# Performance work log

Measured on AMD Instinct MI355X. Metric: run time of the kernel, lower is better.

The kernel has to match this reference:

```python
import jax, jax.numpy as jnp
import numpy as np

N_HEAD = 16


def setup_inputs() -> dict:
    key = jax.random.key(0)
    ks = jax.random.split(key, 6)
    b, l, d = 4, 2048, 1024
    n_mem = 1000  # FAISS index is populated with 1000 random vectors per batch element
    return {
        "q": jax.random.normal(ks[0], (b, l, d), dtype=jnp.float32),
        "kv": jax.random.normal(ks[1], (b, l, d), dtype=jnp.float32),  # unused by forward (faithful)
        "mem_table": jax.random.uniform(ks[2], (b, n_mem, d), dtype=jnp.float32),
        "w_q": jax.random.normal(ks[3], (d, d), dtype=jnp.float32) / np.sqrt(d),
        "w_kv": jax.random.normal(ks[4], (d, 2 * (d // N_HEAD)), dtype=jnp.float32) / np.sqrt(d),
        "w_concat": jax.random.normal(ks[5], (d, d), dtype=jnp.float32) / np.sqrt(d),
        "topk": 1,
    }


def reference(q, kv, mem_table, w_q, w_kv, w_concat, topk):
    b, l, d = q.shape
    h = N_HEAD
    dh = d // h

    qp = q @ w_q  # (b, l, d)

    # Exact inner-product kNN (topk=1) replacing the per-batch FAISS HNSW search:
    # brute-force scores + argmax + gather of the nearest memory vector.
    knn_scores = jnp.einsum("bld,bnd->bln", qp, mem_table)  # (b, l, n_mem)
    idx = jnp.argmax(knn_scores, axis=-1)  # (b, l) int
    mem = jnp.take_along_axis(mem_table, idx[..., None], axis=1)  # (b, l, d)

    k, v = jnp.split(mem @ w_kv, 2, axis=-1)  # each (b, l, dh)

    qh = qp.reshape(b, l, h, dh).transpose(0, 2, 1, 3)  # (b, h, l, dh)
    # k, v are shared across heads (unsqueeze(1) in torch -> broadcast here)
    att = jnp.einsum("bhld,bmd->bhlm", qh, k) / np.float32(np.sqrt(dh))  # (b, h, l, l)
    att = jax.nn.softmax(att, axis=-1)
    out = jnp.einsum("bhlm,bmd->bhld", att, v)  # (b, h, l, dh)

    out = out.transpose(0, 2, 1, 3).reshape(b, l, d)
    return out @ w_concat
```

## Files before the change

kernel.cpp:

```cpp
#include <hip/hip_runtime.h>
#include <float.h>
#include <math.h>

#define BATCH 4
#define SEQ   2048
#define DIM   1024
#define NHEAD 16
#define DHEAD 64
#define NMEM  1000
#define NPAD  1024
#define ROWS  (BATCH*SEQ)
#define QSCALE 0.18033688011112042f

typedef __attribute__((ext_vector_type(8))) __bf16 bf16x8;
typedef __attribute__((ext_vector_type(4))) __bf16 bf16x4;
typedef __attribute__((ext_vector_type(4))) float  f32x4;

static __device__ inline f32x4 mfma16(bf16x8 a, bf16x8 b, f32x4 c) {
  return __builtin_amdgcn_mfma_f32_16x16x32_bf16(a, b, c, 0, 0, 0);
}

#define GLOAD16(g, l) __builtin_amdgcn_global_load_lds( \
    (const __attribute__((address_space(1))) unsigned int*)(g), \
    (__attribute__((address_space(3))) unsigned int*)(l), 16, 0, 0)

enum { MODE_C = 0, MODE_HILO = 1, MODE_ARGMAX = 2, MODE_KV = 3 };

template<int AF32, int NPROD, int MODE>
__global__ __launch_bounds__(256) void gemm3(
    const void* __restrict__ Ah_, const __bf16* __restrict__ Al,
    const __bf16* __restrict__ Bh, const __bf16* __restrict__ Bl,
    int rowsPerZ, long bStrideZ,
    float* __restrict__ C, __bf16* __restrict__ Oh, __bf16* __restrict__ Ol,
    float* __restrict__ pv, int* __restrict__ pi)
{
  extern __shared__ char smem[];
  __shared__ float s_pv[128];
  __shared__ int   s_pi[128];
  const int t = threadIdx.x;
  const int w = t >> 6, lane = t & 63, l15 = lane & 15, g = lane >> 4;
  const int wr = w >> 1, wc = w & 1;
  const int m0 = blockIdx.z * rowsPerZ + blockIdx.x * 128;
  const int n0 = blockIdx.y * 128;
  const __bf16* Bh_b = Bh + (size_t)blockIdx.z * bStrideZ;
  const __bf16* Bl_b = (NPROD == 3) ? (Bl + (size_t)blockIdx.z * bStrideZ) : (const __bf16*)0;

  constexpr int SB = (AF32 || NPROD == 3) ? 32768 : 16384;
  constexpr int BOFF = AF32 ? 16384 : (NPROD == 3 ? 16384 : 8192);

  f32x4 acc[4][4];
  #pragma unroll
  for (int i = 0; i < 4; ++i)
    #pragma unroll
    for (int j = 0; j < 4; ++j) acc[i][j] = (f32x4){0.f, 0.f, 0.f, 0.f};

  auto STAGE = [&](int buf, int k0) {
    char* base = smem + buf * SB;
    if (AF32) {
      const float* Af = (const float*)Ah_;
      #pragma unroll
      for (int i = 0; i < 4; ++i) {
        int c = i * 256 + t;
        int r = c >> 3, s = c & 7;
        int sl = s ^ (r & 7);
        GLOAD16(&Af[(size_t)(m0 + r) * DIM + k0 + sl * 4], base + i * 4096 + w * 1024);
      }
    } else {
      const __bf16* Ab = (const __bf16*)Ah_;
      #pragma unroll
      for (int i = 0; i < 2; ++i) {
        int c = i * 256 + t;
        int r = c >> 2, s = c & 3;
        int sl = s ^ (r & 3);
        GLOAD16(&Ab[(size_t)(m0 + r) * DIM + k0 + sl * 8], base + i * 4096 + w * 1024);
        if (NPROD == 3)
          GLOAD16(&Al[(size_t)(m0 + r) * DIM + k0 + sl * 8], base + 8192 + i * 4096 + w * 1024);
      }
    }
    char* bB = base + BOFF;
    #pragma unroll
    for (int i = 0; i < 2; ++i) {
      int c = i * 256 + t;
      int r = c >> 2, s = c & 3;
      int sl = s ^ (r & 3);
      GLOAD16(&Bh_b[(size_t)(n0 + r) * DIM + k0 + sl * 8], bB + i * 4096 + w * 1024);
      if (NPROD == 3)
        GLOAD16(&Bl_b[(size_t)(n0 + r) * DIM + k0 + sl * 8], bB + 8192 + i * 4096 + w * 1024);
    }
  };

  STAGE(0, 0);
  __syncthreads();
  int cur = 0;

  for (int k0 = 0; k0 < DIM; k0 += 32) {
    if (k0 + 32 < DIM) STAGE(cur ^ 1, k0 + 32);

    char* base = smem + cur * SB;
    char* sA   = base;
    char* sAl  = base + 8192;
    char* sBh  = base + BOFF;
    char* sBl  = sBh + 8192;

    bf16x8 ah[4], al[4], bh[4], bl[4];
    #pragma unroll
    for (int mi = 0; mi < 4; ++mi) {
      int r = wr * 64 + mi * 16 + l15;
      if (AF32) {
        int p0 = (2 * g) ^ (r & 7), p1 = (2 * g + 1) ^ (r & 7);
        float4 q0 = *(const float4*)(sA + r * 128 + p0 * 16);
        float4 q1 = *(const float4*)(sA + r * 128 + p1 * 16);
        float qq[8] = {q0.x, q0.y, q0.z, q0.w, q1.x, q1.y, q1.z, q1.w};
        #pragma unroll
        for (int j = 0; j < 8; ++j) {
          __bf16 h = (__bf16)qq[j];
          ah[mi][j] = h;
          al[mi][j] = (__bf16)(qq[j] - (float)h);
        }
      } else {
        int p = (g ^ (r & 3)) * 16;
        ah[mi] = *(const bf16x8*)(sA + r * 64 + p);
        if (NPROD == 3) al[mi] = *(const bf16x8*)(sAl + r * 64 + p);
      }
    }
    #pragma unroll
    for (int ni = 0; ni < 4; ++ni) {
      int r = wc * 64 + ni * 16 + l15;
      int p = (g ^ (r & 3)) * 16;
      bh[ni] = *(const bf16x8*)(sBh + r * 64 + p);
      if (NPROD == 3) bl[ni] = *(const bf16x8*)(sBl + r * 64 + p);
    }
    __builtin_amdgcn_s_setprio(1);
    #pragma unroll
    for (int mi = 0; mi < 4; ++mi)
      #pragma unroll
      for (int ni = 0; ni < 4; ++ni) {
        acc[mi][ni] = mfma16(ah[mi], bh[ni], acc[mi][ni]);
        if (NPROD == 3) {
          acc[mi][ni] = mfma16(ah[mi], bl[ni], acc[mi][ni]);
          acc[mi][ni] = mfma16(al[mi], bh[ni], acc[mi][ni]);
        }
      }
    __builtin_amdgcn_s_setprio(0);
    __syncthreads();
    cur ^= 1;
  }

  if (MODE == MODE_C) {
    #pragma unroll
    for (int mi = 0; mi < 4; ++mi)
      #pragma unroll
      for (int ni = 0; ni < 4; ++ni) {
        int col = n0 + wc * 64 + ni * 16 + l15;
        #pragma unroll
        for (int r = 0; r < 4; ++r) {
          int row = m0 + wr * 64 + mi * 16 + g * 4 + r;
          C[(size_t)row * DIM + col] = acc[mi][ni][r];
        }
      }
  } else if (MODE == MODE_HILO) {
    #pragma unroll
    for (int mi = 0; mi < 4; ++mi)
      #pragma unroll
      for (int ni = 0; ni < 4; ++ni) {
        int col = n0 + wc * 64 + ni * 16 + l15;
        #pragma unroll
        for (int r = 0; r < 4; ++r) {
          int row = m0 + wr * 64 + mi * 16 + g * 4 + r;
          float v = acc[mi][ni][r] * QSCALE;
          __bf16 h = (__bf16)v;
          Oh[(size_t)row * DIM + col] = h;
          Ol[(size_t)row * DIM + col] = (__bf16)(v - (float)h);
        }
      }
  } else if (MODE == MODE_KV) {
    #pragma unroll
    for (int mi = 0; mi < 4; ++mi)
      #pragma unroll
      for (int ni = 0; ni < 4; ++ni) {
        int col = wc * 64 + ni * 16 + l15;
        #pragma unroll
        for (int r = 0; r < 4; ++r) {
          int gr = m0 + wr * 64 + mi * 16 + g * 4 + r;
          int bb = gr >> 10, n = gr & (NPAD - 1);
          __bf16 h = (__bf16)acc[mi][ni][r];
          if (col < DHEAD) {
            Oh[(size_t)gr * DHEAD + col] = h;
          } else {
            int np = (n & ~63) | ((n & 15) << 2) | ((n >> 4) & 3);
            Ol[((size_t)bb * DHEAD + (col - DHEAD)) * NPAD + np] = h;
          }
        }
      }
  } else {
    float vv[4][4]; int ii[4][4];
    #pragma unroll
    for (int mi = 0; mi < 4; ++mi)
      #pragma unroll
      for (int r = 0; r < 4; ++r) {
        float v = -FLT_MAX; int vi = 0x7fffffff;
        #pragma unroll
        for (int ni = 0; ni < 4; ++ni) {
          int col = n0 + wc * 64 + ni * 16 + l15;
          float s = (col < NMEM) ? acc[mi][ni][r] : -FLT_MAX;
          if (s > v) { v = s; vi = col; }
        }
        #pragma unroll
        for (int off = 1; off < 16; off <<= 1) {
          float ov = __shfl_xor(v, off);
          int   oi = __shfl_xor(vi, off);
          if (ov > v || (ov == v && oi < vi)) { v = ov; vi = oi; }
        }
        vv[mi][r] = v; ii[mi][r] = vi;
        if (wc == 0 && l15 == 0) {
          int lrow = wr * 64 + mi * 16 + g * 4 + r;
          s_pv[lrow] = v; s_pi[lrow] = vi;
        }
      }
    __syncthreads();
    if (wc == 1 && l15 == 0) {
      #pragma unroll
      for (int mi = 0; mi < 4; ++mi)
        #pragma unroll
        for (int r = 0; r < 4; ++r) {
          int lrow = wr * 64 + mi * 16 + g * 4 + r;
          float v0 = s_pv[lrow]; int i0 = s_pi[lrow];
          float v1 = vv[mi][r];  int i1 = ii[mi][r];
          float v; int vi;
          if (v1 > v0) { v = v1; vi = i1; } else { v = v0; vi = i0; }
          pv[(size_t)blockIdx.y * ROWS + m0 + lrow] = v;
          pi[(size_t)blockIdx.y * ROWS + m0 + lrow] = vi;
        }
    }
  }
}

__global__ __launch_bounds__(256) void knn_reduce(const float* __restrict__ pv,
                                                  const int* __restrict__ pi,
                                                  int* __restrict__ idx) {
  int r = blockIdx.x * 256 + threadIdx.x;
  float bv = -FLT_MAX; int bi = 0x7fffffff;
  #pragma unroll
  for (int c = 0; c < 8; ++c) {
    float v = pv[(size_t)c * ROWS + r];
    int   i = pi[(size_t)c * ROWS + r];
    if (v > bv || (v == bv && i < bi)) { bv = v; bi = i; }
  }
  idx[r] = bi;
}

__global__ __launch_bounds__(256) void hist_lc(const int* __restrict__ idx,
                                               float* __restrict__ lc) {
  __shared__ int hcnt[NPAD];
  const int t = threadIdx.x, b = blockIdx.x;
  #pragma unroll
  for (int i = 0; i < 4; ++i) hcnt[t + 256 * i] = 0;
  __syncthreads();
  #pragma unroll
  for (int i = 0; i < 8; ++i) atomicAdd(&hcnt[idx[b * SEQ + i * 256 + t]], 1);
  __syncthreads();
  #pragma unroll
  for (int i = 0; i < 4; ++i) {
    int n = t + 256 * i;
    int c = hcnt[n];
    lc[b * NPAD + n] = (n < NMEM && c > 0) ? log2f((float)c) : -1e30f;
  }
}

__global__ __launch_bounds__(256) void attn_table(const __bf16* __restrict__ qph,
                                                  const __bf16* __restrict__ Ktab,
                                                  const __bf16* __restrict__ VtTp,
                                                  const float* __restrict__ lc2,
                                                  __bf16* __restrict__ attn_bf) {
  extern __shared__ char smem[];
  char* sK = smem;
  char* sV = smem + 16384;
  char* sP = smem + 32768;

  const int t = threadIdx.x;
  const int wq = t >> 6, lane = t & 63, l15 = lane & 15, g = lane >> 4;
  const int b = blockIdx.z, h = blockIdx.y;
  const int q0 = blockIdx.x * 256 + wq * 64;

  bf16x8 qa[4][2];
  #pragma unroll
  for (int mi = 0; mi < 4; ++mi)
    #pragma unroll
    for (int ks = 0; ks < 2; ++ks)
      qa[mi][ks] = *(const bf16x8*)&qph[(size_t)(b * SEQ + q0 + mi * 16 + l15) * DIM +
                                        h * DHEAD + ks * 32 + g * 8];

  f32x4 O[4][4];
  #pragma unroll
  for (int mi = 0; mi < 4; ++mi)
    #pragma unroll
    for (int fd = 0; fd < 4; ++fd) O[mi][fd] = (f32x4){0.f, 0.f, 0.f, 0.f};
  float lsum[4][4];
  #pragma unroll
  for (int mi = 0; mi < 4; ++mi)
    #pragma unroll
    for (int r = 0; r < 4; ++r) lsum[mi][r] = 0.f;

  const __bf16* Kb = Ktab + (size_t)b * NPAD * DHEAD;
  const __bf16* Vb = VtTp + (size_t)b * DHEAD * NPAD;
  const float* lcb = lc2 + b * NPAD;
  char* sPw = sP + wq * 8192;

  auto STAGE = [&](int buf, int tile) {
    const int n0 = tile * 64;
    #pragma unroll
    for (int i = 0; i < 2; ++i) {
      int c = i * 256 + t, row = c >> 3, s = c & 7, sl = s ^ (row & 7);
      GLOAD16(&Kb[(size_t)(n0 + row) * DHEAD + sl * 8], sK + buf * 8192 + i * 4096 + wq * 1024);
      GLOAD16(&Vb[(size_t)row * NPAD + n0 + sl * 8], sV + buf * 8192 + i * 4096 + wq * 1024);
    }
  };

  STAGE(0, 0);
  __syncthreads();
  int cur = 0;

  for (int tile = 0; tile < NPAD / 64; ++tile) {
    if (tile + 1 < NPAD / 64) STAGE(cur ^ 1, tile + 1);

    const int n0 = tile * 64;
    float lcv[4];
    #pragma unroll
    for (int ni = 0; ni < 4; ++ni) lcv[ni] = lcb[n0 + ni * 16 + l15];

    bf16x8 kf[2][4];
    #pragma unroll
    for (int ks = 0; ks < 2; ++ks)
      #pragma unroll
      for (int ni = 0; ni < 4; ++ni)
        kf[ks][ni] = *(const bf16x8*)(sK + cur * 8192 + (ni * 16 + l15) * 128 +
                                      (((ks * 4 + g) ^ (l15 & 7)) * 16));

    #pragma unroll
    for (int mi = 0; mi < 4; ++mi) {
      f32x4 S[4];
      #pragma unroll
      for (int ni = 0; ni < 4; ++ni) S[ni] = (f32x4){0.f, 0.f, 0.f, 0.f};
      __builtin_amdgcn_s_setprio(1);
      #pragma unroll
      for (int ks = 0; ks < 2; ++ks)
        #pragma unroll
        for (int ni = 0; ni < 4; ++ni)
          S[ni] = mfma16(qa[mi][ks], kf[ks][ni], S[ni]);
      __builtin_amdgcn_s_setprio(0);
      #pragma unroll
      for (int r = 0; r < 4; ++r) {
        int row = mi * 16 + g * 4 + r;
        bf16x4 p4;
        float rs = 0.f;
        #pragma unroll
        for (int ni = 0; ni < 4; ++ni) {
          float p = __builtin_amdgcn_exp2f(S[ni][r] + lcv[ni]);
          rs += p;
          p4[ni] = (__bf16)p;
        }
        *(bf16x4*)(sPw + row * 128 + ((l15 * 8) ^ ((row & 7) << 4))) = p4;
        lsum[mi][r] += rs;
      }
    }

    #pragma unroll
    for (int ks = 0; ks < 2; ++ks) {
      bf16x8 vf[4];
      #pragma unroll
      for (int fd = 0; fd < 4; ++fd)
        vf[fd] = *(const bf16x8*)(sV + cur * 8192 + (fd * 16 + l15) * 128 +
                                  (((ks * 4 + g) ^ (l15 & 7)) * 16));
      __builtin_amdgcn_s_setprio(1);
      #pragma unroll
      for (int mi = 0; mi < 4; ++mi) {
        int row = mi * 16 + l15;
        bf16x8 pa = *(const bf16x8*)(sPw + row * 128 +
                                     ((ks * 64 + g * 16) ^ ((row & 7) << 4)));
        #pragma unroll
        for (int fd = 0; fd < 4; ++fd)
          O[mi][fd] = mfma16(pa, vf[fd], O[mi][fd]);
      }
      __builtin_amdgcn_s_setprio(0);
    }

    __syncthreads();
    cur ^= 1;
  }

  #pragma unroll
  for (int mi = 0; mi < 4; ++mi)
    #pragma unroll
    for (int r = 0; r < 4; ++r) {
      float rs = lsum[mi][r];
      #pragma unroll
      for (int off = 1; off < 16; off <<= 1) rs += __shfl_xor(rs, off);
      float inv = 1.f / rs;
      size_t row = (size_t)(b * SEQ + q0 + mi * 16 + g * 4 + r);
      #pragma unroll
      for (int fd = 0; fd < 4; ++fd)
        attn_bf[row * DIM + h * DHEAD + fd * 16 + l15] = (__bf16)(O[mi][fd][r] * inv);
    }
}

__global__ __launch_bounds__(256) void cast_w_t(const float* __restrict__ in,
                                                __bf16* __restrict__ oh,
                                                __bf16* __restrict__ ol,
                                                int writeLo) {
  __shared__ float tile[64][65];
  const int t = threadIdx.x;
  const int k0 = blockIdx.x * 64, n0 = blockIdx.y * 64;
  #pragma unroll
  for (int i = 0; i < 16; ++i) {
    int e = t + i * 256, r = e >> 6, c = e & 63;
    tile[r][c] = in[(size_t)(k0 + r) * DIM + n0 + c];
  }
  __syncthreads();
  #pragma unroll
  for (int i = 0; i < 16; ++i) {
    int e = t + i * 256, r = e >> 6, c = e & 63;
    float v = tile[c][r];
    __bf16 h = (__bf16)v;
    oh[(size_t)(n0 + r) * DIM + k0 + c] = h;
    if (writeLo) ol[(size_t)(n0 + r) * DIM + k0 + c] = (__bf16)(v - (float)h);
  }
}

__global__ __launch_bounds__(256) void cast_wkv_t(const float* __restrict__ in,
                                                  __bf16* __restrict__ oh,
                                                  __bf16* __restrict__ ol) {
  __shared__ float tile[64][65];
  const int t = threadIdx.x;
  const int k0 = blockIdx.x * 64, n0 = blockIdx.y * 64;
  #pragma unroll
  for (int i = 0; i < 16; ++i) {
    int e = t + i * 256, r = e >> 6, c = e & 63;
    tile[r][c] = in[(size_t)(k0 + r) * 128 + n0 + c];
  }
  __syncthreads();
  #pragma unroll
  for (int i = 0; i < 16; ++i) {
    int e = t + i * 256, r = e >> 6, c = e & 63;
    float v = tile[c][r];
    __bf16 h = (__bf16)v;
    oh[(size_t)(n0 + r) * DIM + k0 + c] = h;
    ol[(size_t)(n0 + r) * DIM + k0 + c] = (__bf16)(v - (float)h);
  }
}

__global__ __launch_bounds__(256) void cast_mem(const float* __restrict__ mem,
                                                __bf16* __restrict__ mh,
                                                __bf16* __restrict__ ml) {
  size_t e = ((size_t)blockIdx.x * 256 + threadIdx.x) * 8;
  int d = (int)(e & 1023);
  size_t rn = e >> 10;
  int n = (int)(rn & 1023), b = (int)(rn >> 10);
  bf16x8 h8, l8;
  if (n < NMEM) {
    const float* p = mem + ((size_t)b * NMEM + n) * DIM + d;
    #pragma unroll
    for (int j = 0; j < 8; ++j) {
      float v = p[j];
      __bf16 h = (__bf16)v;
      h8[j] = h; l8[j] = (__bf16)(v - (float)h);
    }
  } else {
    #pragma unroll
    for (int j = 0; j < 8; ++j) { h8[j] = (__bf16)0.f; l8[j] = (__bf16)0.f; }
  }
  *(bf16x8*)(mh + e) = h8;
  *(bf16x8*)(ml + e) = l8;
}

extern "C" void kernel_launch(void* const* d_in, const int* in_sizes, int n_in,
                              void* d_out, int out_size, void* d_ws, size_t ws_size,
                              hipStream_t stream) {
  const float* q        = (const float*)d_in[0];
  const float* mem      = (const float*)d_in[2];
  const float* w_q      = (const float*)d_in[3];
  const float* w_kv     = (const float*)d_in[4];
  const float* w_concat = (const float*)d_in[5];
  float* out = (float*)d_out;

  char* wsb = (char*)d_ws;
  __bf16* memh   = (__bf16*)(wsb + 0);
  __bf16* meml   = (__bf16*)(wsb + 8388608);
  __bf16* wqt_h  = (__bf16*)(wsb + 16777216);
  __bf16* wqt_l  = (__bf16*)(wsb + 18874368);
  __bf16* wct    = (__bf16*)(wsb + 20971520);
  __bf16* Ktab   = (__bf16*)(wsb + 23068672);
  __bf16* VtT    = (__bf16*)(wsb + 23592960);
  float*  lc     = (float*) (wsb + 24117248);
  float*  pv     = (float*) (wsb + 24133632);
  int*    pi     = (int*)   (wsb + 24395776);
  int*    idx    = (int*)   (wsb + 24657920);
  __bf16* wkvT_h = (__bf16*)(wsb + 24690688);
  __bf16* wkvT_l = (__bf16*)(wsb + 24952832);
  __bf16* qph    = (__bf16*)(wsb + 25214976);
  __bf16* qpl    = (__bf16*)(wsb + 41992192);
  __bf16* attn_bf = qpl;

  cast_w_t<<<dim3(16, 16), 256, 0, stream>>>(w_q, wqt_h, wqt_l, 1);
  cast_w_t<<<dim3(16, 16), 256, 0, stream>>>(w_concat, wct, (__bf16*)0, 0);
  cast_wkv_t<<<dim3(16, 2), 256, 0, stream>>>(w_kv, wkvT_h, wkvT_l);
  cast_mem<<<dim3(2048), 256, 0, stream>>>(mem, memh, meml);

  gemm3<1, 3, MODE_HILO><<<dim3(64, 8, 1), 256, 65536, stream>>>(
      (const void*)q, (const __bf16*)0, wqt_h, wqt_l, 0, 0,
      (float*)0, qph, qpl, (float*)0, (int*)0);

  gemm3<0, 3, MODE_KV><<<dim3(BATCH * NPAD / 128, 1, 1), 256, 65536, stream>>>(
      (const void*)memh, meml, wkvT_h, wkvT_l, 0, 0,
      (float*)0, Ktab, VtT, (float*)0, (int*)0);

  gemm3<0, 3, MODE_ARGMAX><<<dim3(16, 8, 4), 256, 65536, stream>>>(
      (const void*)qph, qpl, memh, meml, 2048, (long)NPAD * DIM,
      (float*)0, (__bf16*)0, (__bf16*)0, pv, pi);
  knn_reduce<<<dim3(32), 256, 0, stream>>>(pv, pi, idx);

  hist_lc<<<dim3(BATCH), 256, 0, stream>>>(idx, lc);

  attn_table<<<dim3(SEQ / 256, NHEAD, BATCH), 256, 65536, stream>>>(
      qph, Ktab, VtT, lc, attn_bf);

  gemm3<0, 1, MODE_C><<<dim3(64, 8, 1), 256, 32768, stream>>>(
      (const void*)attn_bf, (const __bf16*)0, wct, (const __bf16*)0, 0, 0,
      out, (__bf16*)0, (__bf16*)0, (float*)0, (int*)0);
}
```

Baseline: 237.2 us.

## Use single-bf16 kNN scoring with top-2 candidates and fp32 rescoring

```diff
diff --git a/kernel.cpp b/kernel.cpp
--- a/kernel.cpp
+++ b/kernel.cpp
@@ -11,6 +11,7 @@
 #define NPAD  1024
 #define ROWS  (BATCH*SEQ)
 #define QSCALE 0.18033688011112042f
+#define RESCORE_DELTA 0.10f
 
 typedef __attribute__((ext_vector_type(8))) __bf16 bf16x8;
 typedef __attribute__((ext_vector_type(4))) __bf16 bf16x4;
@@ -35,8 +36,6 @@
     float* __restrict__ pv, int* __restrict__ pi)
 {
   extern __shared__ char smem[];
-  __shared__ float s_pv[128];
-  __shared__ int   s_pi[128];
   const int t = threadIdx.x;
   const int w = t >> 6, lane = t & 63, l15 = lane & 15, g = lane >> 4;
   const int wr = w >> 1, wc = w & 1;
@@ -193,60 +192,83 @@
         }
       }
   } else {
-    float vv[4][4]; int ii[4][4];
     #pragma unroll
     for (int mi = 0; mi < 4; ++mi)
       #pragma unroll
       for (int r = 0; r < 4; ++r) {
-        float v = -FLT_MAX; int vi = 0x7fffffff;
+        float v1 = -FLT_MAX, v2 = -FLT_MAX;
+        int   i1 = 0x7fffffff, i2 = 0x7fffffff;
         #pragma unroll
         for (int ni = 0; ni < 4; ++ni) {
           int col = n0 + wc * 64 + ni * 16 + l15;
           float s = (col < NMEM) ? acc[mi][ni][r] : -FLT_MAX;
-          if (s > v) { v = s; vi = col; }
+          if (s > v1 || (s == v1 && col < i1)) { v2 = v1; i2 = i1; v1 = s; i1 = col; }
+          else if (s > v2 || (s == v2 && col < i2)) { v2 = s; i2 = col; }
         }
         #pragma unroll
         for (int off = 1; off < 16; off <<= 1) {
-          float ov = __shfl_xor(v, off);
-          int   oi = __shfl_xor(vi, off);
-          if (ov > v || (ov == v && oi < vi)) { v = ov; vi = oi; }
-        }
-        vv[mi][r] = v; ii[mi][r] = vi;
-        if (wc == 0 && l15 == 0) {
-          int lrow = wr * 64 + mi * 16 + g * 4 + r;
-          s_pv[lrow] = v; s_pi[lrow] = vi;
-        }
-      }
-    __syncthreads();
-    if (wc == 1 && l15 == 0) {
-      #pragma unroll
-      for (int mi = 0; mi < 4; ++mi)
-        #pragma unroll
-        for (int r = 0; r < 4; ++r) {
-          int lrow = wr * 64 + mi * 16 + g * 4 + r;
-          float v0 = s_pv[lrow]; int i0 = s_pi[lrow];
-          float v1 = vv[mi][r];  int i1 = ii[mi][r];
-          float v; int vi;
-          if (v1 > v0) { v = v1; vi = i1; } else { v = v0; vi = i0; }
-          pv[(size_t)blockIdx.y * ROWS + m0 + lrow] = v;
-          pi[(size_t)blockIdx.y * ROWS + m0 + lrow] = vi;
-        }
-    }
-  }
-}
-
-__global__ __launch_bounds__(256) void knn_reduce(const float* __restrict__ pv,
-                                                  const int* __restrict__ pi,
-                                                  int* __restrict__ idx) {
-  int r = blockIdx.x * 256 + threadIdx.x;
-  float bv = -FLT_MAX; int bi = 0x7fffffff;
-  #pragma unroll
-  for (int c = 0; c < 8; ++c) {
-    float v = pv[(size_t)c * ROWS + r];
-    int   i = pi[(size_t)c * ROWS + r];
-    if (v > bv || (v == bv && i < bi)) { bv = v; bi = i; }
-  }
-  idx[r] = bi;
+          float w1 = __shfl_xor(v1, off), w2 = __shfl_xor(v2, off);
+          int   j1 = __shfl_xor(i1, off), j2 = __shfl_xor(i2, off);
+          if (w1 > v1 || (w1 == v1 && j1 < i1)) { v2 = v1; i2 = i1; v1 = w1; i1 = j1; }
+          else if (w1 > v2 || (w1 == v2 && j1 < i2)) { v2 = w1; i2 = j1; }
+          if (w2 > v1 || (w2 == v1 && j2 < i1)) { v2 = v1; i2 = i1; v1 = w2; i1 = j2; }
+          else if (w2 > v2 || (w2 == v2 && j2 < i2)) { v2 = w2; i2 = j2; }
+        }
+        if (l15 == 0) {
+          int row = m0 + wr * 64 + mi * 16 + g * 4 + r;
+          int half = blockIdx.y * 2 + wc;
+          pv[(size_t)(half * 2 + 0) * ROWS + row] = v1;
+          pv[(size_t)(half * 2 + 1) * ROWS + row] = v2;
+          pi[(size_t)(half * 2 + 0) * ROWS + row] = i1;
+          pi[(size_t)(half * 2 + 1) * ROWS + row] = i2;
+        }
+      }
+  }
+}
+
+__global__ __launch_bounds__(256) void knn_rescore(const __bf16* __restrict__ qph,
+                                                   const __bf16* __restrict__ qpl,
+                                                   const float* __restrict__ mem,
+                                                   const float* __restrict__ pv,
+                                                   const int* __restrict__ pi,
+                                                   int* __restrict__ idx) {
+  const int t = threadIdx.x;
+  const int wq = t >> 6, lane = t & 63;
+  const int qrow = blockIdx.x * 4 + wq;
+  const int batch = qrow >> 11;
+
+  float cv = (lane < 32) ? pv[(size_t)lane * ROWS + qrow] : -FLT_MAX;
+  int   ci = (lane < 32) ? pi[(size_t)lane * ROWS + qrow] : 0x7fffffff;
+
+  float M = cv;
+  #pragma unroll
+  for (int off = 1; off < 64; off <<= 1) M = fmaxf(M, __shfl_xor(M, off));
+
+  unsigned long long cand = __ballot(cv >= M - RESCORE_DELTA && ci < NMEM);
+
+  float qp[16];
+  {
+    const __bf16* ph = qph + (size_t)qrow * DIM + lane * 16;
+    const __bf16* pl = qpl + (size_t)qrow * DIM + lane * 16;
+    #pragma unroll
+    for (int j = 0; j < 16; ++j) qp[j] = (float)ph[j] + (float)pl[j];
+  }
+
+  float best = -FLT_MAX;
+  int besti = 0x7fffffff;
+  while (cand) {
+    int b = __ffsll((long long)cand) - 1;
+    cand &= cand - 1;
+    int c = __shfl(ci, b);
+    const float* mrow = mem + ((size_t)batch * NMEM + c) * DIM + lane * 16;
+    float part = 0.f;
+    #pragma unroll
+    for (int j = 0; j < 16; ++j) part = fmaf(qp[j], mrow[j], part);
+    #pragma unroll
+    for (int off = 1; off < 64; off <<= 1) part += __shfl_xor(part, off);
+    if (part > best || (part == best && c < besti)) { best = part; besti = c; }
+  }
+  if (lane == 0) idx[qrow] = besti;
 }
 
 __global__ __launch_bounds__(256) void hist_lc(const int* __restrict__ idx,
@@ -472,6 +494,23 @@
   *(bf16x8*)(ml + e) = l8;
 }
 
+__global__ __launch_bounds__(256) void cast_q(const float* __restrict__ q,
+                                              __bf16* __restrict__ qh,
+                                              __bf16* __restrict__ ql) {
+  size_t e = ((size_t)blockIdx.x * 256 + threadIdx.x) * 8;
+  float4 a = *(const float4*)(q + e);
+  float4 b = *(const float4*)(q + e + 4);
+  float vv[8] = {a.x, a.y, a.z, a.w, b.x, b.y, b.z, b.w};
+  bf16x8 h8, l8;
+  #pragma unroll
+  for (int j = 0; j < 8; ++j) {
+    __bf16 h = (__bf16)vv[j];
+    h8[j] = h; l8[j] = (__bf16)(vv[j] - (float)h);
+  }
+  *(bf16x8*)(qh + e) = h8;
+  *(bf16x8*)(ql + e) = l8;
+}
+
 extern "C" void kernel_launch(void* const* d_in, const int* in_sizes, int n_in,
                               void* d_out, int out_size, void* d_ws, size_t ws_size,
                               hipStream_t stream) {
@@ -492,31 +531,35 @@
   __bf16* VtT    = (__bf16*)(wsb + 23592960);
   float*  lc     = (float*) (wsb + 24117248);
   float*  pv     = (float*) (wsb + 24133632);
-  int*    pi     = (int*)   (wsb + 24395776);
-  int*    idx    = (int*)   (wsb + 24657920);
-  __bf16* wkvT_h = (__bf16*)(wsb + 24690688);
-  __bf16* wkvT_l = (__bf16*)(wsb + 24952832);
-  __bf16* qph    = (__bf16*)(wsb + 25214976);
-  __bf16* qpl    = (__bf16*)(wsb + 41992192);
+  int*    pi     = (int*)   (wsb + 25182208);
+  int*    idx    = (int*)   (wsb + 26230784);
+  __bf16* wkvT_h = (__bf16*)(wsb + 26263552);
+  __bf16* wkvT_l = (__bf16*)(wsb + 26525696);
+  __bf16* qph    = (__bf16*)(wsb + 26787840);
+  __bf16* qpl    = (__bf16*)(wsb + 43565056);
   __bf16* attn_bf = qpl;
+  __bf16* qh = (__bf16*)d_out;
+  __bf16* ql = (__bf16*)d_out + (size_t)ROWS * DIM;
 
   cast_w_t<<<dim3(16, 16), 256, 0, stream>>>(w_q, wqt_h, wqt_l, 1);
   cast_w_t<<<dim3(16, 16), 256, 0, stream>>>(w_concat, wct, (__bf16*)0, 0);
   cast_wkv_t<<<dim3(16, 2), 256, 0, stream>>>(w_kv, wkvT_h, wkvT_l);
   cast_mem<<<dim3(2048), 256, 0, stream>>>(mem, memh, meml);
-
-  gemm3<1, 3, MODE_HILO><<<dim3(64, 8, 1), 256, 65536, stream>>>(
-      (const void*)q, (const __bf16*)0, wqt_h, wqt_l, 0, 0,
+  cast_q<<<dim3(4096), 256, 0, stream>>>(q, qh, ql);
+
+  gemm3<0, 3, MODE_HILO><<<dim3(64, 8, 1), 256, 65536, stream>>>(
+      (const void*)qh, ql, wqt_h, wqt_l, 0, 0,
       (float*)0, qph, qpl, (float*)0, (int*)0);
 
   gemm3<0, 3, MODE_KV><<<dim3(BATCH * NPAD / 128, 1, 1), 256, 65536, stream>>>(
       (const void*)memh, meml, wkvT_h, wkvT_l, 0, 0,
       (float*)0, Ktab, VtT, (float*)0, (int*)0);
 
-  gemm3<0, 3, MODE_ARGMAX><<<dim3(16, 8, 4), 256, 65536, stream>>>(
-      (const void*)qph, qpl, memh, meml, 2048, (long)NPAD * DIM,
+  gemm3<0, 1, MODE_ARGMAX><<<dim3(16, 8, 4), 256, 32768, stream>>>(
+      (const void*)qph, (const __bf16*)0, memh, (const __bf16*)0, 2048, (long)NPAD * DIM,
       (float*)0, (__bf16*)0, (__bf16*)0, pv, pi);
-  knn_reduce<<<dim3(32), 256, 0, stream>>>(pv, pi, idx);
+
+  knn_rescore<<<dim3(ROWS / 4), 256, 0, stream>>>(qph, qpl, mem, pv, pi, idx);
 
   hist_lc<<<dim3(BATCH), 256, 0, stream>>>(idx, lc);
 
```

Measured after the change: 241.0 us. Within noise of the previous version (+1.6%).
